# Kernel optimization log

Hardware: AMD Instinct MI355X
Metric: run time of the kernel (lower is better)

The kernel has to match this reference:

```python
import jax, jax.numpy as jnp
import numpy as np

# Staggered-grid first-derivative coefficients (Taylor-optimal), order -> c_1..c_N
_COEFFS = {2: (1.0,),
           4: (9.0 / 8.0, -1.0 / 24.0),
           6: (75.0 / 64.0, -25.0 / 384.0, 3.0 / 640.0),
           8: (1225.0 / 1024.0, -245.0 / 3072.0, 49.0 / 5120.0, -5.0 / 7168.0)}


def _shift(a, s, axis):
    """Zero-padded shift: out[i] = a[i + s] where valid, else 0."""
    if s == 0:
        return a
    nd = a.ndim
    sl = [slice(None)] * nd
    pad = [(0, 0)] * nd
    if s > 0:
        sl[axis] = slice(s, None)
        pad[axis] = (0, s)
    else:
        sl[axis] = slice(None, s)
        pad[axis] = (-s, 0)
    return jnp.pad(a[tuple(sl)], pad)


def _diff1(a, stencil, rd, axis):
    """Integer-grid staggered derivative: sum_k c_k (a[i+k-1] - a[i-k]) * rd."""
    d = jnp.zeros_like(a)
    for k, ck in enumerate(_COEFFS[stencil], start=1):
        d = d + ck * (_shift(a, k - 1, axis) - _shift(a, -k, axis))
    return d * rd


def _diffh1(a, stencil, rd, axis):
    """Half-grid staggered derivative: sum_k c_k (a[i+k] - a[i-k+1]) * rd."""
    d = jnp.zeros_like(a)
    for k, ck in enumerate(_COEFFS[stencil], start=1):
        d = d + ck * (_shift(a, k, axis) - _shift(a, -(k - 1), axis))
    return d * rd


def _step(ca, cb, cq, Ey, Hx, Hz, m_Hx_z, m_Hz_x, m_Ey_x, m_Ey_z,
          ky, ky_h, ay, ay_h, by, by_h, kx, kx_h, ax, ax_h, bx, bx_h,
          rdy, rdx, stencil):
    # ---- update_E ----
    dHz_dx = _diff1(Hz, stencil, rdx, -1)   # d/dx along last axis
    dHx_dz = _diff1(Hx, stencil, rdy, -2)   # d/dz (y) along axis -2
    m_Hz_x = bx * m_Hz_x + ax * dHz_dx
    m_Hx_z = by * m_Hx_z + ay * dHx_dz
    Ey = ca * Ey + cb * ((dHz_dx / kx + m_Hz_x) - (dHx_dz / ky + m_Hx_z))
    # ---- update_H ----
    dEy_dz = _diffh1(Ey, stencil, rdy, -2)
    dEy_dx = _diffh1(Ey, stencil, rdx, -1)
    m_Ey_z = by_h * m_Ey_z + ay_h * dEy_dz
    m_Ey_x = bx_h * m_Ey_x + ax_h * dEy_dx
    Hx = Hx - cq * (dEy_dz / ky_h + m_Ey_z)
    Hz = Hz + cq * (dEy_dx / kx_h + m_Ey_x)
    return jnp.stack([Ey, Hx, Hz, m_Hx_z, m_Hz_x, m_Ey_x, m_Ey_z])


def setup_inputs() -> dict:
    B, NY, NX = 2, 2048, 2048
    key = jax.random.key(0)
    ks = jax.random.split(key, 25)
    f32 = jnp.float32

    def rn(k, s):
        return jax.random.normal(k, s, f32)

    def ru(k, s):
        return jax.random.uniform(k, s, f32)

    inp = {
        'ca': 0.9 + 0.1 * ru(ks[0], (NY, NX)),        # ~1 (low-loss media)
        'cb': 0.1 * ru(ks[1], (NY, NX)),
        'cq': 0.1 * ru(ks[2], (NY, NX)),
        'Ey': rn(ks[3], (B, NY, NX)),
        'Hx': rn(ks[4], (B, NY, NX)),
        'Hz': rn(ks[5], (B, NY, NX)),
        'm_Hx_z': rn(ks[6], (B, NY, NX)),
        'm_Hz_x': rn(ks[7], (B, NY, NX)),
        'm_Ey_x': rn(ks[8], (B, NY, NX)),
        'm_Ey_z': rn(ks[9], (B, NY, NX)),
        'ky': 1.0 + ru(ks[10], (NY, 1)),              # kappa >= 1
        'ky_h': 1.0 + ru(ks[11], (NY, 1)),
        'ay': 0.1 * ru(ks[12], (NY, 1)),
        'ay_h': 0.1 * ru(ks[13], (NY, 1)),
        'by': 0.9 * ru(ks[14], (NY, 1)),
        'by_h': 0.9 * ru(ks[15], (NY, 1)),
        'kx': 1.0 + ru(ks[16], (NX,)),
        'kx_h': 1.0 + ru(ks[17], (NX,)),
        'ax': 0.1 * ru(ks[18], (NX,)),
        'ax_h': 0.1 * ru(ks[19], (NX,)),
        'bx': 0.9 * ru(ks[20], (NX,)),
        'bx_h': 0.9 * ru(ks[21], (NX,)),
        'rdy': jnp.float32(0.1),
        'rdx': jnp.float32(0.1),
        'stencil': 4,
    }
    return inp


def reference(ca, cb, cq, Ey, Hx, Hz, m_Hx_z, m_Hz_x, m_Ey_x, m_Ey_z,
              ky, ky_h, ay, ay_h, by, by_h, kx, kx_h, ax, ax_h, bx, bx_h,
              rdy, rdx, stencil):
    return _step(ca, cb, cq, Ey, Hx, Hz, m_Hx_z, m_Hz_x, m_Ey_x, m_Ey_z,
                 ky, ky_h, ay, ay_h, by, by_h, kx, kx_h, ax, ax_h, bx, bx_h,
                 rdy, rdx, int(stencil))
```

## Files before the change

kernel.cpp:

```cpp
#include <hip/hip_runtime.h>

typedef __attribute__((ext_vector_type(4))) float float4v;

#define TY    8
#define CXW   1024
#define CXP   (CXW + 8)
#define NSLOT 8

__device__ __forceinline__ float4v ld4(const float* __restrict__ p) {
    return *(const float4v*)p;
}
__device__ __forceinline__ void st4(float* __restrict__ p, float4v v) {
    *(float4v*)p = v;
}
__device__ __forceinline__ float frcp(float x) {
    return __builtin_amdgcn_rcpf(x);
}

__device__ __forceinline__ void getC(int st, float C[4]) {
    C[0] = 1.f; C[1] = 0.f; C[2] = 0.f; C[3] = 0.f;
    if (st == 4)      { C[0] = 1.125f;          C[1] = -1.f / 24.f; }
    else if (st == 6) { C[0] = 75.f / 64.f;     C[1] = -25.f / 384.f;
                        C[2] = 3.f / 640.f; }
    else if (st == 8) { C[0] = 1225.f / 1024.f; C[1] = -245.f / 3072.f;
                        C[2] = 49.f / 5120.f;   C[3] = -5.f / 7168.f; }
}

__global__ __launch_bounds__(256) void fdtd_fused(
    const float* __restrict__ ca,   const float* __restrict__ cb,
    const float* __restrict__ cq,
    const float* __restrict__ Ey,   const float* __restrict__ Hx,
    const float* __restrict__ Hz,
    const float* __restrict__ mHxz, const float* __restrict__ mHzx,
    const float* __restrict__ mEyx, const float* __restrict__ mEyz,
    const float* __restrict__ ky,   const float* __restrict__ kyh,
    const float* __restrict__ ay,   const float* __restrict__ ayh,
    const float* __restrict__ by,   const float* __restrict__ byh,
    const float* __restrict__ kx,   const float* __restrict__ kxh,
    const float* __restrict__ ax,   const float* __restrict__ axh,
    const float* __restrict__ bx,   const float* __restrict__ bxh,
    const float* __restrict__ rdyp, const float* __restrict__ rdxp,
    const int* __restrict__ stp,
    float* __restrict__ outEy,   float* __restrict__ outHx,
    float* __restrict__ outHz,   float* __restrict__ outMHxz,
    float* __restrict__ outMHzx, float* __restrict__ outMEyx,
    float* __restrict__ outMEyz,
    int B, int NY, int NX, int NSTRIP, int NCHUNK)
{
    __shared__ float eyl[NSLOT][CXP];

    const int nwg = NSTRIP * NCHUNK;
    int idx = blockIdx.x;
    if ((nwg & 7) == 0) {
        const int q = nwg >> 3;
        idx = (idx & 7) * q + (idx >> 3);
    }
    const int strip = idx % NSTRIP;
    const int chunk = idx / NSTRIP;
    const int b   = blockIdx.y;
    const int y0  = strip * TY;
    const int X0  = chunk * CXW;

    const int tid = (int)threadIdx.x;
    const int x0  = X0 + tid * 4;
    const int lc0 = tid * 4;

    const float rdx = rdxp[0];
    const float rdy = rdyp[0];
    int ns = stp[0] >> 1;
    if (ns < 1) ns = 1; if (ns > 4) ns = 4;
    float C[4]; getC(ns * 2, C);

    const size_t NXs = (size_t)NX;
    const size_t planeOff = (size_t)b * (size_t)NY * NXs;
    const float4v z4 = {0.f, 0.f, 0.f, 0.f};

    float4v kxhv = z4, axhv = z4, bxhv = z4, rkxh = z4;
    if (x0 + 4 <= NX) {
        kxhv = ld4(kxh + x0); axhv = ld4(axh + x0); bxhv = ld4(bxh + x0);
        #pragma unroll
        for (int i = 0; i < 4; ++i) rkxh[i] = frcp(kxhv[i]);
    }

    auto computeE = [&](int r, int xb, bool wr,
                        float ayv, float byv, float rky) -> float4v {
        if (r < 0 || r >= NY || xb < 0 || xb >= NX) return z4;
        const size_t rb = planeOff + (size_t)r * NXs;
        float w[12];
        {
            float4v l0 = (xb >= 4)       ? ld4(Hz + rb + (xb - 4)) : z4;
            float4v l1 =                   ld4(Hz + rb + xb);
            float4v l2 = (xb + 8 <= NX)  ? ld4(Hz + rb + xb + 4)   : z4;
            w[0]=l0.x; w[1]=l0.y; w[2] =l0.z; w[3] =l0.w;
            w[4]=l1.x; w[5]=l1.y; w[6] =l1.z; w[7] =l1.w;
            w[8]=l2.x; w[9]=l2.y; w[10]=l2.z; w[11]=l2.w;
        }
        float dzx[4] = {0.f,0.f,0.f,0.f}, dxz[4] = {0.f,0.f,0.f,0.f};
        #pragma unroll
        for (int k = 1; k <= 4; ++k) {
            if (k <= ns) {
                const float ck = C[k - 1];
                #pragma unroll
                for (int i = 0; i < 4; ++i)
                    dzx[i] += ck * (w[i + 3 + k] - w[i + 4 - k]);
                const int yp = r + k - 1, ym = r - k;
                float4v up = (yp < NY) ? ld4(Hx + rb + (size_t)(k - 1) * NXs + xb) : z4;
                float4v dn = (ym >= 0) ? ld4(Hx + rb - (size_t)k * NXs + xb)       : z4;
                #pragma unroll
                for (int i = 0; i < 4; ++i)
                    dxz[i] += ck * (up[i] - dn[i]);
            }
        }
        const size_t cr = (size_t)r * NXs + (size_t)xb;
        float4v eyv = ld4(Ey   + rb + xb);
        float4v mzx = ld4(mHzx + rb + xb);
        float4v mxz = ld4(mHxz + rb + xb);
        float4v cav = ld4(ca + cr);
        float4v cbv = ld4(cb + cr);
        float4v kxv = ld4(kx + xb);
        float4v axv = ld4(ax + xb);
        float4v bxv = ld4(bx + xb);
        float4v oE, oMxz, oMzx;
        #pragma unroll
        for (int i = 0; i < 4; ++i) {
            const float dHzdx = dzx[i] * rdx;
            const float dHxdz = dxz[i] * rdy;
            const float mzx_n = bxv[i] * mzx[i] + axv[i] * dHzdx;
            const float mxz_n = byv    * mxz[i] + ayv    * dHxdz;
            oE[i] = cav[i] * eyv[i]
                  + cbv[i] * ((dHzdx * frcp(kxv[i]) + mzx_n)
                            - (dHxdz * rky          + mxz_n));
            oMxz[i] = mxz_n;
            oMzx[i] = mzx_n;
        }
        if (wr) {
            st4(outEy   + rb + xb, oE);
            st4(outMHxz + rb + xb, oMxz);
            st4(outMHzx + rb + xb, oMzx);
        }
        return oE;
    };

    for (int e = 1 - ns; e < TY + ns; ++e) {
        const int r = y0 + e;
        float ayv = 0.f, byv = 0.f, rky = 0.f;
        if (r >= 0 && r < NY) {
            ayv = ay[r]; byv = by[r]; rky = frcp(ky[r]);
        }
        const bool wr = (e >= 0) && (e < TY);
        float4v eM = computeE(r, x0, wr, ayv, byv, rky);
        float4v eL = z4, eR = z4;
        if (tid == 0 && X0 >= 4)
            eL = computeE(r, X0 - 4, false, ayv, byv, rky);
        if (tid == 255 && X0 + CXW < NX)
            eR = computeE(r, X0 + CXW, false, ayv, byv, rky);

        __syncthreads();
        const int slot = r & (NSLOT - 1);
        st4(&eyl[slot][lc0 + 4], eM);
        if (tid == 0)   st4(&eyl[slot][0],        eL);
        if (tid == 255) st4(&eyl[slot][CXW + 4],  eR);
        __syncthreads();

        if (e >= ns) {
            const int h = r - ns;
            if (h < NY && x0 + 4 <= NX) {
                const size_t rb = planeOff + (size_t)h * NXs;
                const int hs = h & (NSLOT - 1);
                float lw[12];
                {
                    float4v a0 = ld4(&eyl[hs][lc0]);
                    float4v a1 = ld4(&eyl[hs][lc0 + 4]);
                    float4v a2 = ld4(&eyl[hs][lc0 + 8]);
                    lw[0]=a0.x; lw[1]=a0.y; lw[2] =a0.z; lw[3] =a0.w;
                    lw[4]=a1.x; lw[5]=a1.y; lw[6] =a1.z; lw[7] =a1.w;
                    lw[8]=a2.x; lw[9]=a2.y; lw[10]=a2.z; lw[11]=a2.w;
                }
                float dEdx[4] = {0.f,0.f,0.f,0.f}, dEdz[4] = {0.f,0.f,0.f,0.f};
                #pragma unroll
                for (int k = 1; k <= 4; ++k) {
                    if (k <= ns) {
                        const float ck = C[k - 1];
                        #pragma unroll
                        for (int i = 0; i < 4; ++i)
                            dEdx[i] += ck * (lw[i + 4 + k] - lw[i + 5 - k]);
                        float4v up = ld4(&eyl[(h + k)     & (NSLOT - 1)][lc0 + 4]);
                        float4v dn = ld4(&eyl[(h - k + 1) & (NSLOT - 1)][lc0 + 4]);
                        #pragma unroll
                        for (int i = 0; i < 4; ++i)
                            dEdz[i] += ck * (up[i] - dn[i]);
                    }
                }
                float4v hxv = ld4(Hx   + rb + x0);
                float4v hzv = ld4(Hz   + rb + x0);
                float4v mxv = ld4(mEyx + rb + x0);
                float4v mzv = ld4(mEyz + rb + x0);
                float4v cqv = ld4(cq + (size_t)h * NXs + x0);
                const float ayhv = ayh[h];
                const float byhv = byh[h];
                const float rkyh = frcp(kyh[h]);
                float4v oHx, oHz, oMx, oMz;
                #pragma unroll
                for (int i = 0; i < 4; ++i) {
                    const float dz = dEdz[i] * rdy;
                    const float dx = dEdx[i] * rdx;
                    const float mz_n = byhv    * mzv[i] + ayhv    * dz;
                    const float mx_n = bxhv[i] * mxv[i] + axhv[i] * dx;
                    oHx[i] = hxv[i] - cqv[i] * (dz * rkyh    + mz_n);
                    oHz[i] = hzv[i] + cqv[i] * (dx * rkxh[i] + mx_n);
                    oMx[i] = mx_n;
                    oMz[i] = mz_n;
                }
                st4(outHx   + rb + x0, oHx);
                st4(outHz   + rb + x0, oHz);
                st4(outMEyx + rb + x0, oMx);
                st4(outMEyz + rb + x0, oMz);
            }
        }
    }
}

extern "C" void kernel_launch(void* const* d_in, const int* in_sizes, int n_in,
                              void* d_out, int out_size, void* d_ws, size_t ws_size,
                              hipStream_t stream)
{
    const float* ca   = (const float*)d_in[0];
    const float* cb   = (const float*)d_in[1];
    const float* cq   = (const float*)d_in[2];
    const float* Ey   = (const float*)d_in[3];
    const float* Hx   = (const float*)d_in[4];
    const float* Hz   = (const float*)d_in[5];
    const float* mHxz = (const float*)d_in[6];
    const float* mHzx = (const float*)d_in[7];
    const float* mEyx = (const float*)d_in[8];
    const float* mEyz = (const float*)d_in[9];
    const float* ky   = (const float*)d_in[10];
    const float* kyh  = (const float*)d_in[11];
    const float* ay   = (const float*)d_in[12];
    const float* ayh  = (const float*)d_in[13];
    const float* by   = (const float*)d_in[14];
    const float* byh  = (const float*)d_in[15];
    const float* kx   = (const float*)d_in[16];
    const float* kxh  = (const float*)d_in[17];
    const float* ax   = (const float*)d_in[18];
    const float* axh  = (const float*)d_in[19];
    const float* bx   = (const float*)d_in[20];
    const float* bxh  = (const float*)d_in[21];
    const float* rdy  = (const float*)d_in[22];
    const float* rdx  = (const float*)d_in[23];
    const int*   stp  = (const int*)d_in[24];

    const int NX   = in_sizes[16];
    const int NYNX = in_sizes[0];
    const int NY   = NYNX / NX;
    const int B    = in_sizes[3] / NYNX;
    const size_t plane = (size_t)B * (size_t)NYNX;

    float* out     = (float*)d_out;
    float* outEy   = out;
    float* outHx   = out + 1 * plane;
    float* outHz   = out + 2 * plane;
    float* outMHxz = out + 3 * plane;
    float* outMHzx = out + 4 * plane;
    float* outMEyx = out + 5 * plane;
    float* outMEyz = out + 6 * plane;

    const int NSTRIP = (NY + TY - 1) / TY;
    const int NCHUNK = (NX + CXW - 1) / CXW;

    dim3 grid(NSTRIP * NCHUNK, B);
    dim3 block(256);

    fdtd_fused<<<grid, block, 0, stream>>>(
        ca, cb, cq, Ey, Hx, Hz, mHxz, mHzx, mEyx, mEyz,
        ky, kyh, ay, ayh, by, byh, kx, kxh, ax, axh, bx, bxh,
        rdy, rdx, stp,
        outEy, outHx, outHz, outMHxz, outMHzx, outMEyx, outMEyz,
        B, NY, NX, NSTRIP, NCHUNK);
}
```

Before: 501.4 us.

## Shrink tiles to 128 threads, template ring size, prefetch H-update loads

```diff
diff --git a/kernel.cpp b/kernel.cpp
--- a/kernel.cpp
+++ b/kernel.cpp
@@ -2,10 +2,10 @@
 
 typedef __attribute__((ext_vector_type(4))) float float4v;
 
-#define TY    8
-#define CXW   1024
+#define TY    4
+#define CXW   512
 #define CXP   (CXW + 8)
-#define NSLOT 8
+#define NTHR  128
 
 __device__ __forceinline__ float4v ld4(const float* __restrict__ p) {
     return *(const float4v*)p;
@@ -26,7 +26,8 @@
                         C[2] = 49.f / 5120.f;   C[3] = -5.f / 7168.f; }
 }
 
-__global__ __launch_bounds__(256) void fdtd_fused(
+template<int NSLOT, int NSMIN, int NSMAX>
+__global__ __launch_bounds__(NTHR, 6) void fdtd_fused(
     const float* __restrict__ ca,   const float* __restrict__ cb,
     const float* __restrict__ cq,
     const float* __restrict__ Ey,   const float* __restrict__ Hx,
@@ -47,6 +48,10 @@
     float* __restrict__ outMEyz,
     int B, int NY, int NX, int NSTRIP, int NCHUNK)
 {
+    int ns = stp[0] >> 1;
+    if (ns < 1) ns = 1; if (ns > 4) ns = 4;
+    if (ns < NSMIN || ns > NSMAX) return;
+
     __shared__ float eyl[NSLOT][CXP];
 
     const int nwg = NSTRIP * NCHUNK;
@@ -67,8 +72,6 @@
 
     const float rdx = rdxp[0];
     const float rdy = rdyp[0];
-    int ns = stp[0] >> 1;
-    if (ns < 1) ns = 1; if (ns > 4) ns = 4;
     float C[4]; getC(ns * 2, C);
 
     const size_t NXs = (size_t)NX;
@@ -143,79 +146,84 @@
 
     for (int e = 1 - ns; e < TY + ns; ++e) {
         const int r = y0 + e;
+        const int h = r - ns;
+        const bool doH = (e >= ns) && (h < NY) && (x0 + 4 <= NX);
+
+        float4v hxv = z4, hzv = z4, mxv = z4, mzv = z4, cqv = z4;
+        float ayhv = 0.f, byhv = 0.f, rkyh = 0.f;
+        size_t hb = 0;
+        if (doH) {
+            hb  = planeOff + (size_t)h * NXs;
+            hxv = ld4(Hx   + hb + x0);
+            hzv = ld4(Hz   + hb + x0);
+            mxv = ld4(mEyx + hb + x0);
+            mzv = ld4(mEyz + hb + x0);
+            cqv = ld4(cq + (size_t)h * NXs + x0);
+            ayhv = ayh[h];
+            byhv = byh[h];
+            rkyh = frcp(kyh[h]);
+        }
+
         float ayv = 0.f, byv = 0.f, rky = 0.f;
         if (r >= 0 && r < NY) {
             ayv = ay[r]; byv = by[r]; rky = frcp(ky[r]);
         }
         const bool wr = (e >= 0) && (e < TY);
         float4v eM = computeE(r, x0, wr, ayv, byv, rky);
-        float4v eL = z4, eR = z4;
-        if (tid == 0 && X0 >= 4)
-            eL = computeE(r, X0 - 4, false, ayv, byv, rky);
-        if (tid == 255 && X0 + CXW < NX)
-            eR = computeE(r, X0 + CXW, false, ayv, byv, rky);
+        float4v eH = z4;
+        if (tid < 2) {
+            const int xh = (tid == 0) ? X0 - 4 : X0 + CXW;
+            eH = computeE(r, xh, false, ayv, byv, rky);
+        }
 
         __syncthreads();
         const int slot = r & (NSLOT - 1);
         st4(&eyl[slot][lc0 + 4], eM);
-        if (tid == 0)   st4(&eyl[slot][0],        eL);
-        if (tid == 255) st4(&eyl[slot][CXW + 4],  eR);
+        if (tid < 2) st4(&eyl[slot][tid == 0 ? 0 : CXW + 4], eH);
         __syncthreads();
 
-        if (e >= ns) {
-            const int h = r - ns;
-            if (h < NY && x0 + 4 <= NX) {
-                const size_t rb = planeOff + (size_t)h * NXs;
-                const int hs = h & (NSLOT - 1);
-                float lw[12];
-                {
-                    float4v a0 = ld4(&eyl[hs][lc0]);
-                    float4v a1 = ld4(&eyl[hs][lc0 + 4]);
-                    float4v a2 = ld4(&eyl[hs][lc0 + 8]);
-                    lw[0]=a0.x; lw[1]=a0.y; lw[2] =a0.z; lw[3] =a0.w;
-                    lw[4]=a1.x; lw[5]=a1.y; lw[6] =a1.z; lw[7] =a1.w;
-                    lw[8]=a2.x; lw[9]=a2.y; lw[10]=a2.z; lw[11]=a2.w;
+        if (doH) {
+            const int hs = h & (NSLOT - 1);
+            float lw[12];
+            {
+                float4v a0 = ld4(&eyl[hs][lc0]);
+                float4v a1 = ld4(&eyl[hs][lc0 + 4]);
+                float4v a2 = ld4(&eyl[hs][lc0 + 8]);
+                lw[0]=a0.x; lw[1]=a0.y; lw[2] =a0.z; lw[3] =a0.w;
+                lw[4]=a1.x; lw[5]=a1.y; lw[6] =a1.z; lw[7] =a1.w;
+                lw[8]=a2.x; lw[9]=a2.y; lw[10]=a2.z; lw[11]=a2.w;
+            }
+            float dEdx[4] = {0.f,0.f,0.f,0.f}, dEdz[4] = {0.f,0.f,0.f,0.f};
+            #pragma unroll
+            for (int k = 1; k <= 4; ++k) {
+                if (k <= ns) {
+                    const float ck = C[k - 1];
+                    #pragma unroll
+                    for (int i = 0; i < 4; ++i)
+                        dEdx[i] += ck * (lw[i + 4 + k] - lw[i + 5 - k]);
+                    float4v up = ld4(&eyl[(h + k)     & (NSLOT - 1)][lc0 + 4]);
+                    float4v dn = ld4(&eyl[(h - k + 1) & (NSLOT - 1)][lc0 + 4]);
+                    #pragma unroll
+                    for (int i = 0; i < 4; ++i)
+                        dEdz[i] += ck * (up[i] - dn[i]);
                 }
-                float dEdx[4] = {0.f,0.f,0.f,0.f}, dEdz[4] = {0.f,0.f,0.f,0.f};
-                #pragma unroll
-                for (int k = 1; k <= 4; ++k) {
-                    if (k <= ns) {
-                        const float ck = C[k - 1];
-                        #pragma unroll
-                        for (int i = 0; i < 4; ++i)
-                            dEdx[i] += ck * (lw[i + 4 + k] - lw[i + 5 - k]);
-                        float4v up = ld4(&eyl[(h + k)     & (NSLOT - 1)][lc0 + 4]);
-                        float4v dn = ld4(&eyl[(h - k + 1) & (NSLOT - 1)][lc0 + 4]);
-                        #pragma unroll
-                        for (int i = 0; i < 4; ++i)
-                            dEdz[i] += ck * (up[i] - dn[i]);
-                    }
-                }
-                float4v hxv = ld4(Hx   + rb + x0);
-                float4v hzv = ld4(Hz   + rb + x0);
-                float4v mxv = ld4(mEyx + rb + x0);
-                float4v mzv = ld4(mEyz + rb + x0);
-                float4v cqv = ld4(cq + (size_t)h * NXs + x0);
-                const float ayhv = ayh[h];
-                const float byhv = byh[h];
-                const float rkyh = frcp(kyh[h]);
-                float4v oHx, oHz, oMx, oMz;
-                #pragma unroll
-                for (int i = 0; i < 4; ++i) {
-                    const float dz = dEdz[i] * rdy;
-                    const float dx = dEdx[i] * rdx;
-                    const float mz_n = byhv    * mzv[i] + ayhv    * dz;
-                    const float mx_n = bxhv[i] * mxv[i] + axhv[i] * dx;
-                    oHx[i] = hxv[i] - cqv[i] * (dz * rkyh    + mz_n);
-                    oHz[i] = hzv[i] + cqv[i] * (dx * rkxh[i] + mx_n);
-                    oMx[i] = mx_n;
-                    oMz[i] = mz_n;
-                }
-                st4(outHx   + rb + x0, oHx);
-                st4(outHz   + rb + x0, oHz);
-                st4(outMEyx + rb + x0, oMx);
-                st4(outMEyz + rb + x0, oMz);
-            }
+            }
+            float4v oHx, oHz, oMx, oMz;
+            #pragma unroll
+            for (int i = 0; i < 4; ++i) {
+                const float dz = dEdz[i] * rdy;
+                const float dx = dEdx[i] * rdx;
+                const float mz_n = byhv    * mzv[i] + ayhv    * dz;
+                const float mx_n = bxhv[i] * mxv[i] + axhv[i] * dx;
+                oHx[i] = hxv[i] - cqv[i] * (dz * rkyh    + mz_n);
+                oHz[i] = hzv[i] + cqv[i] * (dx * rkxh[i] + mx_n);
+                oMx[i] = mx_n;
+                oMz[i] = mz_n;
+            }
+            st4(outHx   + hb + x0, oHx);
+            st4(outHz   + hb + x0, oHz);
+            st4(outMEyx + hb + x0, oMx);
+            st4(outMEyz + hb + x0, oMz);
         }
     }
 }
@@ -269,12 +277,19 @@
     const int NCHUNK = (NX + CXW - 1) / CXW;
 
     dim3 grid(NSTRIP * NCHUNK, B);
-    dim3 block(256);
-
-    fdtd_fused<<<grid, block, 0, stream>>>(
+    dim3 block(NTHR);
+
+    fdtd_fused<4, 1, 2><<<grid, block, 0, stream>>>(
         ca, cb, cq, Ey, Hx, Hz, mHxz, mHzx, mEyx, mEyz,
         ky, kyh, ay, ayh, by, byh, kx, kxh, ax, axh, bx, bxh,
         rdy, rdx, stp,
         outEy, outHx, outHz, outMHxz, outMHzx, outMEyx, outMEyz,
         B, NY, NX, NSTRIP, NCHUNK);
-}
+
+    fdtd_fused<8, 3, 4><<<grid, block, 0, stream>>>(
+        ca, cb, cq, Ey, Hx, Hz, mHxz, mHzx, mEyx, mEyz,
+        ky, kyh, ay, ayh, by, byh, kx, kxh, ax, axh, bx, bxh,
+        rdy, rdx, stp,
+        outEy, outHx, outHz, outMHxz, outMHzx, outMEyx, outMEyz,
+        B, NY, NX, NSTRIP, NCHUNK);
+}
```

Result: slower. 696.0 us (+38.8%).
